# Optimization experiments

Hardware: AMD Instinct MI355X
Metric: run time of the kernel (lower is better)

## Reference

```python
import jax, jax.numpy as jnp
import numpy as np

N = 30000      # paper nodes
E = 300000     # edges per etype
IN = 128       # in_feats
HID = 128      # n_hidden
H, D = 4, 32   # n_heads, head dim (HID // H)
C = 16         # n_classes
T = 2          # n_etypes
SLOPE = 0.2    # GATConv leaky-relu negative slope


def setup_inputs() -> dict:
    key = jax.random.key(0)
    ks = jax.random.split(key, 24)
    def w(k, shape, fan):
        return jax.random.normal(k, shape, jnp.float32) * (fan ** -0.5)
    inp = {}
    inp["x"] = jax.random.normal(ks[0], (N, IN), jnp.float32)
    inp["src0"] = jax.random.randint(ks[1], (E,), 0, N, jnp.int32)
    inp["dst0"] = jax.random.randint(ks[2], (E,), 0, N, jnp.int32)
    inp["src1"] = jax.random.randint(ks[3], (E,), 0, N, jnp.int32)
    inp["dst1"] = jax.random.randint(ks[4], (E,), 0, N, jnp.int32)
    # layer 1: in_feats -> H*D, per etype (stacked on leading etype axis)
    inp["W1"]  = w(ks[5], (T, IN, H * D), IN)
    inp["al1"] = w(ks[6], (T, H, D), D)
    inp["ar1"] = w(ks[7], (T, H, D), D)
    inp["b1"]  = jnp.zeros((T, H * D), jnp.float32)
    # layers 2,3: HID -> H*D
    inp["W2"]  = w(ks[8], (T, HID, H * D), HID)
    inp["al2"] = w(ks[9], (T, H, D), D)
    inp["ar2"] = w(ks[10], (T, H, D), D)
    inp["b2"]  = jnp.zeros((T, H * D), jnp.float32)
    inp["W3"]  = w(ks[11], (T, HID, H * D), HID)
    inp["al3"] = w(ks[12], (T, H, D), D)
    inp["ar3"] = w(ks[13], (T, H, D), D)
    inp["b3"]  = jnp.zeros((T, H * D), jnp.float32)
    # output linear
    inp["Wout"] = w(ks[14], (HID, C), HID)
    inp["bout"] = jnp.zeros((C,), jnp.float32)
    return inp


def _gat(h, src, dst, W, al, ar, b):
    """Single-etype GATConv. h:[N,F], W:[F,H*D], al/ar:[H,D], b:[H*D] -> [N,H,D]."""
    feat = (h @ W).reshape(N, H, D)                       # [N,H,D]
    el = jnp.sum(feat * al, axis=-1)                      # [N,H]
    er = jnp.sum(feat * ar, axis=-1)                      # [N,H]
    e = jax.nn.leaky_relu(el[src] + er[dst], SLOPE)       # [E,H]
    # edge softmax over incoming edges of each dst node, per head
    m = jax.ops.segment_max(e, dst, num_segments=N)       # [N,H]
    ex = jnp.exp(e - m[dst])                              # [E,H]
    s = jax.ops.segment_sum(ex, dst, num_segments=N)      # [N,H]
    alpha = ex / s[dst]                                   # [E,H]
    msg = feat[src] * alpha[:, :, None]                   # [E,H,D]
    out = jax.ops.segment_sum(msg, dst, num_segments=N)   # [N,H,D]
    return out + b.reshape(1, H, D)


def _hetero_layer(h, srcs, dsts, W, al, ar, b):
    # HeteroGraphConv: sum-aggregate GATConv outputs across etypes, then flatten heads
    out = _gat(h, srcs[0], dsts[0], W[0], al[0], ar[0], b[0])
    for t in range(1, T):
        out = out + _gat(h, srcs[t], dsts[t], W[t], al[t], ar[t], b[t])
    return out.reshape(N, H * D)


def reference(x, src0, dst0, src1, dst1,
              W1, al1, ar1, b1, W2, al2, ar2, b2, W3, al3, ar3, b3,
              Wout, bout):
    srcs, dsts = (src0, src1), (dst0, dst1)
    h = _hetero_layer(x, srcs, dsts, W1, al1, ar1, b1)
    h = jax.nn.relu(h)  # dropout omitted (eval mode)
    h = _hetero_layer(h, srcs, dsts, W2, al2, ar2, b2)
    h = jax.nn.relu(h)
    h = _hetero_layer(h, srcs, dsts, W3, al3, ar3, b3)
    return h @ Wout + bout  # [N, C]
```

## Files before the change

kernel.cpp:

```cpp
#include <hip/hip_runtime.h>

#define NN 30000
#define EE 300000
#define HH 4
#define SLOPE 0.2f
#define SCAN_NB 15

typedef _Float16 f16;
typedef f16 f16x8 __attribute__((ext_vector_type(8)));
typedef float f32x4 __attribute__((ext_vector_type(4)));

__global__ __launch_bounds__(256) void prep_k(const float* __restrict__ W0,
                                              const float* __restrict__ W1,
                                              const float* __restrict__ W2,
                                              f16* __restrict__ Wh,
                                              int4* __restrict__ deg4) {
    const int z = blockIdx.z;
    if (z == 3) {
        const int base = (blockIdx.y * 8 + blockIdx.x) * 256 + threadIdx.x;
        for (int j = base; j < 2 * NN / 4; j += 4096) deg4[j] = make_int4(0, 0, 0, 0);
        return;
    }
    const int t = blockIdx.y;
    const float* W = (z == 0) ? W0 : ((z == 1) ? W1 : W2);
    f16* Whl = Wh + (size_t)z * 2 * 16384;
    const int i0 = blockIdx.x * 2048;
    #pragma unroll
    for (int j = 0; j < 8; ++j) {
        const int i = i0 + threadIdx.x + j * 256;
        const int k = i >> 7, col = i & 127;
        Whl[t * 16384 + col * 128 + k] = (f16)W[t * 16384 + i];
    }
}

#define APAD 136
__global__ __launch_bounds__(256) void gemm_mfma(const f16* __restrict__ Ah,
                                                 const float* __restrict__ Af,
                                                 const int use_f32,
                                                 const f16* __restrict__ Whbase,
                                                 const float* __restrict__ albase,
                                                 const float* __restrict__ arbase,
                                                 f16* __restrict__ featbase,
                                                 float* __restrict__ elbase,
                                                 float* __restrict__ erbase) {
    __shared__ f16 Bsl[128 * APAD];
    const int bx = blockIdx.x >> 1;
    const int et = blockIdx.x & 1;
    const f16* Wh = Whbase + et * 16384;
    f16* feat = featbase + (size_t)et * NN * 128;
    const int row0 = bx * 64;
    const int t = threadIdx.x;

    #pragma unroll
    for (int j = 0; j < 8; ++j) {
        const int idx = t + j * 256;
        const int col = idx >> 4, k16 = idx & 15;
        *reinterpret_cast<float4*>(&Bsl[col * APAD + k16 * 8]) =
            *reinterpret_cast<const float4*>(Wh + col * 128 + k16 * 8);
    }
    __syncthreads();

    const int w = t >> 6, lane = t & 63;
    const int r = lane & 15, g = lane >> 4;
    const int mb = w * 16;
    const int rowa = min(row0 + mb + r, NN - 1);
    f32x4 acc[8];
    #pragma unroll
    for (int nt = 0; nt < 8; ++nt) acc[nt] = (f32x4){0.f, 0.f, 0.f, 0.f};

    #pragma unroll
    for (int ks = 0; ks < 4; ++ks) {
        f16x8 av;
        if (use_f32) {
            const float4 a0 =
                *reinterpret_cast<const float4*>(Af + (size_t)rowa * 128 + ks * 32 + g * 8);
            const float4 a1 =
                *reinterpret_cast<const float4*>(Af + (size_t)rowa * 128 + ks * 32 + g * 8 + 4);
            av[0] = (f16)a0.x; av[1] = (f16)a0.y; av[2] = (f16)a0.z; av[3] = (f16)a0.w;
            av[4] = (f16)a1.x; av[5] = (f16)a1.y; av[6] = (f16)a1.z; av[7] = (f16)a1.w;
        } else {
            av = *reinterpret_cast<const f16x8*>(Ah + (size_t)rowa * 128 + ks * 32 + g * 8);
        }
        #pragma unroll
        for (int nt = 0; nt < 8; ++nt) {
            const f16x8 bv =
                *reinterpret_cast<const f16x8*>(&Bsl[(nt * 16 + r) * APAD + ks * 32 + g * 8]);
            acc[nt] = __builtin_amdgcn_mfma_f32_16x16x32_f16(av, bv, acc[nt], 0, 0, 0);
        }
    }

    float alv[8], arv[8];
    #pragma unroll
    for (int nt = 0; nt < 8; ++nt) {
        alv[nt] = albase[et * 128 + nt * 16 + r];
        arv[nt] = arbase[et * 128 + nt * 16 + r];
    }
    #pragma unroll
    for (int p = 0; p < 4; ++p) {
        const int row = row0 + mb + g * 4 + p;
        const bool ok = row < NN;
        if (ok) {
            #pragma unroll
            for (int nt = 0; nt < 8; ++nt)
                feat[(size_t)row * 128 + nt * 16 + r] = (f16)acc[nt][p];
        }
        #pragma unroll
        for (int h = 0; h < 4; ++h) {
            float pl = fmaf(acc[2 * h][p], alv[2 * h], acc[2 * h + 1][p] * alv[2 * h + 1]);
            float pr = fmaf(acc[2 * h][p], arv[2 * h], acc[2 * h + 1][p] * arv[2 * h + 1]);
            pl += __shfl_xor(pl, 1); pl += __shfl_xor(pl, 2);
            pl += __shfl_xor(pl, 4); pl += __shfl_xor(pl, 8);
            pr += __shfl_xor(pr, 1); pr += __shfl_xor(pr, 2);
            pr += __shfl_xor(pr, 4); pr += __shfl_xor(pr, 8);
            if (ok && r == 0) {
                elbase[et * NN * HH + row * HH + h] = pl;
                erbase[et * NN * HH + row * HH + h] = pr;
            }
        }
    }
}

__global__ __launch_bounds__(256) void hist4_k(const int* __restrict__ dst0,
                                               const int* __restrict__ dst1,
                                               int* __restrict__ deg) {
    const int i = blockIdx.x * 256 + threadIdx.x;
    if (i >= EE / 4) return;
    const int t = blockIdx.y;
    const int4 d = reinterpret_cast<const int4*>(t ? dst1 : dst0)[i];
    int* dg = deg + t * NN;
    atomicAdd(&dg[d.x], 1);
    atomicAdd(&dg[d.y], 1);
    atomicAdd(&dg[d.z], 1);
    atomicAdd(&dg[d.w], 1);
}

__global__ __launch_bounds__(256) void scan1_k(const int* __restrict__ deg,
                                               int* __restrict__ offs,
                                               int* __restrict__ blocksum) {
    const int t = blockIdx.y, b = blockIdx.x;
    const int* d = deg + t * NN;
    int* o = offs + t * (NN + 1);
    const int base = b * 2048 + threadIdx.x * 8;
    int v[8];
    int s = 0;
    #pragma unroll
    for (int j = 0; j < 8; ++j) {
        const int i = base + j;
        v[j] = (i < NN) ? d[i] : 0;
        s += v[j];
    }
    __shared__ int buf[256];
    buf[threadIdx.x] = s;
    __syncthreads();
    #pragma unroll
    for (int ofs = 1; ofs < 256; ofs <<= 1) {
        const int add = (threadIdx.x >= (unsigned)ofs) ? buf[threadIdx.x - ofs] : 0;
        __syncthreads();
        buf[threadIdx.x] += add;
        __syncthreads();
    }
    int run = buf[threadIdx.x] - s;
    #pragma unroll
    for (int j = 0; j < 8; ++j) {
        const int i = base + j;
        if (i < NN) o[i] = run;
        run += v[j];
    }
    if (threadIdx.x == 255) blocksum[t * SCAN_NB + b] = buf[255];
}

__global__ __launch_bounds__(256) void scan3b_k(int* __restrict__ offs,
                                                const int* __restrict__ blocksum,
                                                int* __restrict__ cursor) {
    const int t = blockIdx.y, b = blockIdx.x;
    int boff = 0;
    #pragma unroll
    for (int i = 0; i < SCAN_NB; ++i)
        if (i < b) boff += blocksum[t * SCAN_NB + i];
    int* o = offs + t * (NN + 1);
    int* cur = cursor + t * NN;
    if (b == SCAN_NB - 1 && threadIdx.x == 0)
        o[NN] = boff + blocksum[t * SCAN_NB + SCAN_NB - 1];
    const int base = b * 2048 + threadIdx.x * 8;
    #pragma unroll
    for (int j = 0; j < 8; ++j) {
        const int i = base + j;
        if (i < NN) {
            const int val = o[i] + boff;
            o[i] = val;
            cur[i] = val;
        }
    }
}

__global__ __launch_bounds__(256) void scatter4_k(const int* __restrict__ src0,
                                                  const int* __restrict__ dst0,
                                                  const int* __restrict__ src1,
                                                  const int* __restrict__ dst1,
                                                  int* __restrict__ cursor,
                                                  int* __restrict__ csr_src) {
    const int i = blockIdx.x * 256 + threadIdx.x;
    if (i >= EE / 4) return;
    const int t = blockIdx.y;
    const int4 s = reinterpret_cast<const int4*>(t ? src1 : src0)[i];
    const int4 d = reinterpret_cast<const int4*>(t ? dst1 : dst0)[i];
    int* cur = cursor + t * NN;
    int* cs = csr_src + t * EE;
    cs[atomicAdd(&cur[d.x], 1)] = s.x;
    cs[atomicAdd(&cur[d.y], 1)] = s.y;
    cs[atomicAdd(&cur[d.z], 1)] = s.z;
    cs[atomicAdd(&cur[d.w], 1)] = s.w;
}

__global__ __launch_bounds__(256) void pull_agg9_k(const int* __restrict__ csr_src,
                                                   const int* __restrict__ offs,
                                                   const float* __restrict__ el,
                                                   const float* __restrict__ er,
                                                   const f16* __restrict__ feat,
                                                   const float* __restrict__ b0,
                                                   const float* __restrict__ b1,
                                                   f16* __restrict__ out, int relu) {
    __shared__ float xb[2][2][128];
    const int w = threadIdx.x >> 6, lane = threadIdx.x & 63;
    const int p = w >> 1, t = w & 1;
    const int n = blockIdx.x * 2 + p;
    const int sub = lane >> 4;
    const int cg = lane & 15;
    const int h = cg >> 2;
    const int c0 = cg * 8;

    const int* so = offs + t * (NN + 1);
    const int e0 = so[n], e1 = so[n + 1];

    float s = 0.f;
    float x[8];
    #pragma unroll
    for (int j = 0; j < 8; ++j) x[j] = 0.f;

    if (e0 < e1) {
        const int* cs = csr_src + t * EE;
        const float* elt = el + t * NN * HH;
        const float erh = er[t * NN * HH + n * HH + h];
        const f16* ft = feat + (size_t)t * NN * 128;
        const int elast = e1 - 1;

        int si_0 = cs[min(e0 + sub, elast)];
        int si_1 = cs[min(e0 + 4 + sub, elast)];
        int si_2 = cs[min(e0 + 8 + sub, elast)];
        float lv_0 = elt[si_0 * HH + h];
        f16x8 fr_0 = *reinterpret_cast<const f16x8*>(ft + (size_t)si_0 * 128 + c0);
        float lv_1 = elt[si_1 * HH + h];
        f16x8 fr_1 = *reinterpret_cast<const f16x8*>(ft + (size_t)si_1 * 128 + c0);

        for (int eb = e0; eb < e1; eb += 4) {
            const int si_3 = cs[min(eb + 12 + sub, elast)];
            const float lv_2 = elt[si_2 * HH + h];
            const f16x8 fr_2 = *reinterpret_cast<const f16x8*>(ft + (size_t)si_2 * 128 + c0);
            float v = lv_0 + erh;
            v = (v >= 0.f) ? v : v * SLOPE;
            float ex = __expf(v);
            ex = (eb + sub < e1) ? ex : 0.f;
            s += ex;
            #pragma unroll
            for (int j = 0; j < 8; ++j) x[j] = fmaf(ex, (float)fr_0[j], x[j]);
            lv_0 = lv_1; fr_0 = fr_1;
            lv_1 = lv_2; fr_1 = fr_2;
            si_2 = si_3;
        }
    }

    s += __shfl_xor(s, 16); s += __shfl_xor(s, 32);
    #pragma unroll
    for (int j = 0; j < 8; ++j) {
        x[j] += __shfl_xor(x[j], 16);
        x[j] += __shfl_xor(x[j], 32);
    }
    const float inv = (s > 0.f) ? 1.f / s : 0.f;
    if (sub == 0) {
        float4 v0 = make_float4(x[0] * inv, x[1] * inv, x[2] * inv, x[3] * inv);
        float4 v1 = make_float4(x[4] * inv, x[5] * inv, x[6] * inv, x[7] * inv);
        *reinterpret_cast<float4*>(&xb[p][t][c0]) = v0;
        *reinterpret_cast<float4*>(&xb[p][t][c0 + 4]) = v1;
    }
    __syncthreads();
    if (t == 0) {
        const int c = lane * 2;
        float a0 = xb[p][0][c] + xb[p][1][c] + b0[c] + b1[c];
        float a1 = xb[p][0][c + 1] + xb[p][1][c + 1] + b0[c + 1] + b1[c + 1];
        if (relu) { a0 = fmaxf(a0, 0.f); a1 = fmaxf(a1, 0.f); }
        union { f16 h2[2]; float f; } o;
        o.h2[0] = (f16)a0; o.h2[1] = (f16)a1;
        *reinterpret_cast<float*>(out + (size_t)n * 128 + c) = o.f;
    }
}

__global__ __launch_bounds__(256) void out_gemm_k(const f16* __restrict__ A,
                                                  const float* __restrict__ W,
                                                  const float* __restrict__ bout,
                                                  float* __restrict__ out) {
    __shared__ float At[16][132];
    const int row0 = blockIdx.x * 16;
    const int t = threadIdx.x;
    {
        const int r = t >> 4, c8 = t & 15;
        const f16x8 v = *reinterpret_cast<const f16x8*>(A + (size_t)(row0 + r) * 128 + c8 * 8);
        #pragma unroll
        for (int j = 0; j < 8; ++j) At[r][c8 * 8 + j] = (float)v[j];
    }
    __syncthreads();
    const int r = t >> 4, c = t & 15;
    float accv = 0.f;
    #pragma unroll 8
    for (int k = 0; k < 128; ++k) accv = fmaf(At[r][k], W[k * 16 + c], accv);
    out[(row0 + r) * 16 + c] = accv + bout[c];
}

extern "C" void kernel_launch(void* const* d_in, const int* in_sizes, int n_in,
                              void* d_out, int out_size, void* d_ws, size_t ws_size,
                              hipStream_t stream) {
    (void)in_sizes; (void)n_in; (void)out_size; (void)ws_size;
    const float* x = (const float*)d_in[0];
    const int* src0 = (const int*)d_in[1];
    const int* dst0 = (const int*)d_in[2];
    const int* src1 = (const int*)d_in[3];
    const int* dst1 = (const int*)d_in[4];
    const float* W[3]  = {(const float*)d_in[5], (const float*)d_in[9],  (const float*)d_in[13]};
    const float* al[3] = {(const float*)d_in[6], (const float*)d_in[10], (const float*)d_in[14]};
    const float* ar[3] = {(const float*)d_in[7], (const float*)d_in[11], (const float*)d_in[15]};
    const float* bb[3] = {(const float*)d_in[8], (const float*)d_in[12], (const float*)d_in[16]};
    const float* Wout = (const float*)d_in[17];
    const float* bout = (const float*)d_in[18];
    float* outp = (float*)d_out;

    char* pb = (char*)d_ws;
    f16* feat   = (f16*)pb;    pb += (size_t)2 * NN * 128 * 2;
    f16* hbuf   = (f16*)pb;    pb += (size_t)NN * 128 * 2;
    float* el   = (float*)pb;  pb += (size_t)2 * NN * HH * 4;
    float* er   = (float*)pb;  pb += (size_t)2 * NN * HH * 4;
    int* deg    = (int*)pb;    pb += (size_t)2 * NN * 4;
    int* cursor = (int*)pb;    pb += (size_t)2 * NN * 4;
    int* offs   = (int*)pb;    pb += (size_t)2 * (NN + 1) * 4;
    int* bsum   = (int*)pb;    pb += (size_t)2 * SCAN_NB * 4;
    f16* Wh     = (f16*)pb;    pb += (size_t)3 * 2 * 128 * 128 * 2;
    int* csr    = (int*)pb;    pb += (size_t)2 * EE * 4;

    prep_k<<<dim3(8, 2, 4), 256, 0, stream>>>(W[0], W[1], W[2], Wh, (int4*)deg);
    hist4_k<<<dim3((EE / 4 + 255) / 256, 2), 256, 0, stream>>>(dst0, dst1, deg);
    scan1_k<<<dim3(SCAN_NB, 2), 256, 0, stream>>>(deg, offs, bsum);
    scan3b_k<<<dim3(SCAN_NB, 2), 256, 0, stream>>>(offs, bsum, cursor);
    scatter4_k<<<dim3((EE / 4 + 255) / 256, 2), 256, 0, stream>>>(src0, dst0, src1, dst1,
                                                                  cursor, csr);

    const f16* hin = hbuf;
    for (int l = 0; l < 3; ++l) {
        gemm_mfma<<<938, 256, 0, stream>>>(
            hin, x, (l == 0) ? 1 : 0, Wh + l * 2 * 16384, al[l], ar[l], feat, el, er);
        pull_agg9_k<<<NN / 2, 256, 0, stream>>>(csr, offs, el, er, feat,
                                                bb[l], bb[l] + 128, hbuf, (l < 2) ? 1 : 0);
        hin = hbuf;
    }
    out_gemm_k<<<NN / 16, 256, 0, stream>>>(hbuf, Wout, bout, outp);
}
```

Measured before the change: 227.7 us.

## Fuse output linear into last aggregation and predicate out-of-range edge gathers

The final 128x16 output projection now runs inside the layer-3 aggregation kernel. The aggregated row goes to shared memory and is multiplied by Wout with a shuffle reduction, so the separate out_gemm kernel and the fp16 round trip of the last hidden state are gone. Prefetched gathers past the end of a node's edge list are now predicated off instead of clamped to the last edge, which avoids redundant loads. This costs an extra barrier and more register pressure in the aggregation kernel.

```diff
diff --git a/kernel.cpp b/kernel.cpp
--- a/kernel.cpp
+++ b/kernel.cpp
@@ -212,14 +212,17 @@
     cs[atomicAdd(&cur[d.w], 1)] = s.w;
 }
 
-__global__ __launch_bounds__(256) void pull_agg9_k(const int* __restrict__ csr_src,
-                                                   const int* __restrict__ offs,
-                                                   const float* __restrict__ el,
-                                                   const float* __restrict__ er,
-                                                   const f16* __restrict__ feat,
-                                                   const float* __restrict__ b0,
-                                                   const float* __restrict__ b1,
-                                                   f16* __restrict__ out, int relu) {
+__global__ __launch_bounds__(256) void pull_agg10_k(const int* __restrict__ csr_src,
+                                                    const int* __restrict__ offs,
+                                                    const float* __restrict__ el,
+                                                    const float* __restrict__ er,
+                                                    const f16* __restrict__ feat,
+                                                    const float* __restrict__ b0,
+                                                    const float* __restrict__ b1,
+                                                    f16* __restrict__ out, int relu,
+                                                    const float* __restrict__ Wout,
+                                                    const float* __restrict__ bout,
+                                                    float* __restrict__ outf, int fuse_out) {
     __shared__ float xb[2][2][128];
     const int w = threadIdx.x >> 6, lane = threadIdx.x & 63;
     const int p = w >> 1, t = w & 1;
@@ -242,30 +245,45 @@
         const float* elt = el + t * NN * HH;
         const float erh = er[t * NN * HH + n * HH + h];
         const f16* ft = feat + (size_t)t * NN * 128;
-        const int elast = e1 - 1;
-
-        int si_0 = cs[min(e0 + sub, elast)];
-        int si_1 = cs[min(e0 + 4 + sub, elast)];
-        int si_2 = cs[min(e0 + 8 + sub, elast)];
-        float lv_0 = elt[si_0 * HH + h];
-        f16x8 fr_0 = *reinterpret_cast<const f16x8*>(ft + (size_t)si_0 * 128 + c0);
-        float lv_1 = elt[si_1 * HH + h];
-        f16x8 fr_1 = *reinterpret_cast<const f16x8*>(ft + (size_t)si_1 * 128 + c0);
+
+        bool v0 = (e0 + sub) < e1;
+        bool v1 = (e0 + 4 + sub) < e1;
+        bool v2 = (e0 + 8 + sub) < e1;
+        int si_0 = 0, si_1 = 0, si_2 = 0;
+        if (v0) si_0 = cs[e0 + sub];
+        if (v1) si_1 = cs[e0 + 4 + sub];
+        if (v2) si_2 = cs[e0 + 8 + sub];
+        float lv_0 = 0.f, lv_1 = 0.f;
+        f16x8 fr_0 = {}, fr_1 = {};
+        if (v0) {
+            lv_0 = elt[si_0 * HH + h];
+            fr_0 = *reinterpret_cast<const f16x8*>(ft + (size_t)si_0 * 128 + c0);
+        }
+        if (v1) {
+            lv_1 = elt[si_1 * HH + h];
+            fr_1 = *reinterpret_cast<const f16x8*>(ft + (size_t)si_1 * 128 + c0);
+        }
 
         for (int eb = e0; eb < e1; eb += 4) {
-            const int si_3 = cs[min(eb + 12 + sub, elast)];
-            const float lv_2 = elt[si_2 * HH + h];
-            const f16x8 fr_2 = *reinterpret_cast<const f16x8*>(ft + (size_t)si_2 * 128 + c0);
+            const bool v3 = (eb + 12 + sub) < e1;
+            int si_3 = 0;
+            if (v3) si_3 = cs[eb + 12 + sub];
+            float lv_2 = 0.f;
+            f16x8 fr_2 = {};
+            if (v2) {
+                lv_2 = elt[si_2 * HH + h];
+                fr_2 = *reinterpret_cast<const f16x8*>(ft + (size_t)si_2 * 128 + c0);
+            }
             float v = lv_0 + erh;
             v = (v >= 0.f) ? v : v * SLOPE;
             float ex = __expf(v);
-            ex = (eb + sub < e1) ? ex : 0.f;
+            ex = v0 ? ex : 0.f;
             s += ex;
             #pragma unroll
             for (int j = 0; j < 8; ++j) x[j] = fmaf(ex, (float)fr_0[j], x[j]);
-            lv_0 = lv_1; fr_0 = fr_1;
-            lv_1 = lv_2; fr_1 = fr_2;
-            si_2 = si_3;
+            lv_0 = lv_1; fr_0 = fr_1; v0 = v1;
+            lv_1 = lv_2; fr_1 = fr_2; v1 = v2;
+            si_2 = si_3; v2 = v3;
         }
     }
 
@@ -277,42 +295,40 @@
     }
     const float inv = (s > 0.f) ? 1.f / s : 0.f;
     if (sub == 0) {
-        float4 v0 = make_float4(x[0] * inv, x[1] * inv, x[2] * inv, x[3] * inv);
-        float4 v1 = make_float4(x[4] * inv, x[5] * inv, x[6] * inv, x[7] * inv);
-        *reinterpret_cast<float4*>(&xb[p][t][c0]) = v0;
-        *reinterpret_cast<float4*>(&xb[p][t][c0 + 4]) = v1;
+        float4 v0s = make_float4(x[0] * inv, x[1] * inv, x[2] * inv, x[3] * inv);
+        float4 v1s = make_float4(x[4] * inv, x[5] * inv, x[6] * inv, x[7] * inv);
+        *reinterpret_cast<float4*>(&xb[p][t][c0]) = v0s;
+        *reinterpret_cast<float4*>(&xb[p][t][c0 + 4]) = v1s;
     }
     __syncthreads();
     if (t == 0) {
         const int c = lane * 2;
         float a0 = xb[p][0][c] + xb[p][1][c] + b0[c] + b1[c];
         float a1 = xb[p][0][c + 1] + xb[p][1][c + 1] + b0[c + 1] + b1[c + 1];
-        if (relu) { a0 = fmaxf(a0, 0.f); a1 = fmaxf(a1, 0.f); }
-        union { f16 h2[2]; float f; } o;
-        o.h2[0] = (f16)a0; o.h2[1] = (f16)a1;
-        *reinterpret_cast<float*>(out + (size_t)n * 128 + c) = o.f;
-    }
-}
-
-__global__ __launch_bounds__(256) void out_gemm_k(const f16* __restrict__ A,
-                                                  const float* __restrict__ W,
-                                                  const float* __restrict__ bout,
-                                                  float* __restrict__ out) {
-    __shared__ float At[16][132];
-    const int row0 = blockIdx.x * 16;
-    const int t = threadIdx.x;
-    {
-        const int r = t >> 4, c8 = t & 15;
-        const f16x8 v = *reinterpret_cast<const f16x8*>(A + (size_t)(row0 + r) * 128 + c8 * 8);
+        if (!fuse_out) {
+            if (relu) { a0 = fmaxf(a0, 0.f); a1 = fmaxf(a1, 0.f); }
+            union { f16 h2[2]; float f; } o;
+            o.h2[0] = (f16)a0; o.h2[1] = (f16)a1;
+            *reinterpret_cast<float*>(out + (size_t)n * 128 + c) = o.f;
+        } else {
+            xb[p][0][c] = a0;
+            xb[p][0][c + 1] = a1;
+        }
+    }
+    if (fuse_out) {
+        __syncthreads();
+        const int p2 = threadIdx.x >> 7;
+        const int c = (threadIdx.x >> 3) & 15;
+        const int j = threadIdx.x & 7;
+        float acc = 0.f;
         #pragma unroll
-        for (int j = 0; j < 8; ++j) At[r][c8 * 8 + j] = (float)v[j];
-    }
-    __syncthreads();
-    const int r = t >> 4, c = t & 15;
-    float accv = 0.f;
-    #pragma unroll 8
-    for (int k = 0; k < 128; ++k) accv = fmaf(At[r][k], W[k * 16 + c], accv);
-    out[(row0 + r) * 16 + c] = accv + bout[c];
+        for (int k = 0; k < 16; ++k) {
+            const int kk = j * 16 + k;
+            acc = fmaf(xb[p2][0][kk], Wout[kk * 16 + c], acc);
+        }
+        acc += __shfl_xor(acc, 1); acc += __shfl_xor(acc, 2); acc += __shfl_xor(acc, 4);
+        if (j == 0) outf[(size_t)(blockIdx.x * 2 + p2) * 16 + c] = acc + bout[c];
+    }
 }
 
 extern "C" void kernel_launch(void* const* d_in, const int* in_sizes, int n_in,
@@ -355,9 +371,9 @@
     for (int l = 0; l < 3; ++l) {
         gemm_mfma<<<938, 256, 0, stream>>>(
             hin, x, (l == 0) ? 1 : 0, Wh + l * 2 * 16384, al[l], ar[l], feat, el, er);
-        pull_agg9_k<<<NN / 2, 256, 0, stream>>>(csr, offs, el, er, feat,
-                                                bb[l], bb[l] + 128, hbuf, (l < 2) ? 1 : 0);
+        pull_agg10_k<<<NN / 2, 256, 0, stream>>>(csr, offs, el, er, feat,
+                                                 bb[l], bb[l] + 128, hbuf, (l < 2) ? 1 : 0,
+                                                 Wout, bout, outp, (l == 2) ? 1 : 0);
         hin = hbuf;
     }
-    out_gemm_k<<<NN / 16, 256, 0, stream>>>(hbuf, Wout, bout, outp);
-}
+}
```

Result: slower. 267.8 us (+17.6%).
